# Kernel tuning notes

Hardware: AMD Instinct MI355X
Metric: run time of the kernel (lower is better)

## Reference

```python
import jax, jax.numpy as jnp
import numpy as np

N = 50000
E = 640000
IN_DIM = 128
HIDDEN = 128
OUT_DIM = 128


def setup_inputs() -> dict:
    key = jax.random.key(0)
    ks = jax.random.split(key, 8)
    x = jax.random.normal(ks[0], (N, IN_DIM), dtype=jnp.float32)
    edge_index = jax.random.randint(ks[1], (2, E), 0, N, dtype=jnp.int64)
    s = 1.0 / np.sqrt(IN_DIM)
    w1l = jax.random.uniform(ks[2], (HIDDEN, IN_DIM), minval=-s, maxval=s, dtype=jnp.float32)
    b1 = jax.random.uniform(ks[3], (HIDDEN,), minval=-s, maxval=s, dtype=jnp.float32)
    w1r = jax.random.uniform(ks[4], (HIDDEN, IN_DIM), minval=-s, maxval=s, dtype=jnp.float32)
    s2 = 1.0 / np.sqrt(HIDDEN)
    w2l = jax.random.uniform(ks[5], (OUT_DIM, HIDDEN), minval=-s2, maxval=s2, dtype=jnp.float32)
    b2 = jax.random.uniform(ks[6], (OUT_DIM,), minval=-s2, maxval=s2, dtype=jnp.float32)
    w2r = jax.random.uniform(ks[7], (OUT_DIM, HIDDEN), minval=-s2, maxval=s2, dtype=jnp.float32)
    return {"x": x, "edge_index": edge_index, "w1l": w1l, "b1": b1, "w1r": w1r,
            "w2l": w2l, "b2": b2, "w2r": w2r}


def sage_conv(x, src, dst, wl, bl, wr):
    # mean-aggregate source features at destination nodes
    msg = x[src]                                   # [E, d]
    agg = jax.ops.segment_sum(msg, dst, num_segments=N)   # [N, d]
    cnt = jax.ops.segment_sum(jnp.ones((src.shape[0],), x.dtype), dst, num_segments=N)
    agg = agg / jnp.maximum(cnt, 1.0)[:, None]
    # PyG SAGEConv: lin_l(agg) + lin_r(x); bias lives in lin_l
    return agg @ wl.T + bl + x @ wr.T


def reference(x, edge_index, w1l, b1, w1r, w2l, b2, w2r):
    src, dst = edge_index[0], edge_index[1]
    h = jax.nn.relu(sage_conv(x, src, dst, w1l, b1, w1r))
    out = sage_conv(h, src, dst, w2l, b2, w2r)
    return out
```

## Files before the change

### kernel.cpp

```cpp
#include <hip/hip_runtime.h>

#define DIM 128
#define CAP 64
#define FSTRIDE 16
#define PBLK 320

typedef _Float16 half8 __attribute__((ext_vector_type(8)));
typedef float floatx4 __attribute__((ext_vector_type(4)));
typedef unsigned short ushort8 __attribute__((ext_vector_type(8)));

__global__ void k_setup(const floatx4* __restrict__ in4, half8* __restrict__ out8,
                        const float* __restrict__ w1l, const float* __restrict__ w1r,
                        half8* __restrict__ Wf1,
                        const float* __restrict__ w2l, const float* __restrict__ w2r,
                        half8* __restrict__ Wf2,
                        const int* __restrict__ src, const int* __restrict__ dst,
                        int* __restrict__ fillS, unsigned short* __restrict__ pad,
                        int n8, int N, int E){
  int b = blockIdx.x;
  if (b < 8*PBLK){
    const int p = b & 7, c = b >> 3;
    const int PN = (N + 7) >> 3;
    const int n0 = p * PN;
    const int n1 = (n0 + PN < N) ? n0 + PN : N;
    const int CE = (E + PBLK - 1) / PBLK;
    const int e0 = c * CE;
    const int e1 = (e0 + CE < E) ? e0 + CE : E;
    for (int e = e0 + threadIdx.x; e < e1; e += 256){
      int d = dst[e];
      if (d >= n0 && d < n1){
        int s = src[e];
        int q = atomicAdd(&fillS[d*FSTRIDE], 1);
        if (q < CAP) pad[d*CAP + q] = (unsigned short)s;
      }
    }
  } else if (b < 8*PBLK + ((n8 + 255) >> 8)){
    int i = (b - 8*PBLK)*256 + threadIdx.x;
    if (i < n8){
      floatx4 a = in4[2*i], c = in4[2*i + 1];
      half8 h;
      h[0] = (_Float16)a[0]; h[1] = (_Float16)a[1];
      h[2] = (_Float16)a[2]; h[3] = (_Float16)a[3];
      h[4] = (_Float16)c[0]; h[5] = (_Float16)c[1];
      h[6] = (_Float16)c[2]; h[7] = (_Float16)c[3];
      out8[i] = h;
    }
  } else {
    int which = b - 8*PBLK - ((n8 + 255) >> 8);
    const float* wl = (which < 16) ? w1l : w2l;
    const float* wr = (which < 16) ? w1r : w2r;
    half8* Wf = (which < 16) ? Wf1 : Wf2;
    int t = (which & 15)*256 + threadIdx.x;
    int ks = t >> 9, jt = (t >> 6) & 7, lane = t & 63;
    int j = jt*16 + (lane & 15);
    int kb = ks*32 + (lane >> 4)*8;
    half8 h;
    #pragma unroll
    for (int i = 0; i < 8; ++i){
      int k = kb + i;
      float v = (k < 128) ? wl[j*128 + k] : wr[j*128 + (k - 128)];
      h[i] = (_Float16)v;
    }
    Wf[t] = h;
  }
}

__global__ __launch_bounds__(256) void k_agg(
    const half8* __restrict__ featH8, const unsigned short* __restrict__ pad,
    const int* __restrict__ fillS, half8* __restrict__ aggH8, int n)
{
  int node = blockIdx.x*16 + (threadIdx.x >> 4);
  int ch = threadIdx.x & 15;
  if (node >= n) return;
  int deg = fillS[node*FSTRIDE];
  int cnt = (deg < CAP) ? deg : CAP;
  const int base = node*CAP;
  float acc[8] = {0,0,0,0,0,0,0,0};
  for (int p = 0; p < cnt; p += 8){
    ushort8 si = *(const ushort8*)&pad[base + p];
    int   s[8];
    float w[8];
    #pragma unroll
    for (int u = 0; u < 8; ++u){
      bool valid = (p + u) < cnt;
      s[u] = valid ? (int)si[u] : 0;
      w[u] = valid ? 1.0f : 0.0f;
    }
    half8 v[8];
    #pragma unroll
    for (int u = 0; u < 8; ++u) v[u] = featH8[s[u]*16 + ch];
    #pragma unroll
    for (int u = 0; u < 8; ++u){
      #pragma unroll
      for (int i = 0; i < 8; ++i) acc[i] += w[u] * (float)v[u][i];
    }
  }
  float sc = 1.0f / fmaxf((float)deg, 1.0f);
  half8 o;
  #pragma unroll
  for (int i = 0; i < 8; ++i) o[i] = (_Float16)(acc[i]*sc);
  aggH8[node*16 + ch] = o;
}

template<bool RELU, bool OUT_HALF>
__global__ __launch_bounds__(256) void k_gemm(
    const half8* __restrict__ aggH8, const half8* __restrict__ selfH8,
    const half8* __restrict__ Wf, const float* __restrict__ bias,
    void* __restrict__ outp, int n)
{
  const int tid = threadIdx.x;
  const int lane = tid & 63, wv = tid >> 6;
  const int m = lane & 15, quad = lane >> 4;
  const int node0 = blockIdx.x * 64;
  const int arow = node0 + wv*16 + m;
  const int rowSafe = (arow < n) ? arow : 0;

  floatx4 acc[8] = {{0,0,0,0},{0,0,0,0},{0,0,0,0},{0,0,0,0},
                    {0,0,0,0},{0,0,0,0},{0,0,0,0},{0,0,0,0}};

  #pragma unroll
  for (int ks = 0; ks < 8; ++ks){
    half8 a = (ks < 4) ? aggH8 [rowSafe*16 + (ks    *4 + quad)]
                       : selfH8[rowSafe*16 + ((ks-4)*4 + quad)];
    if (arow >= n) a = half8{};
    #pragma unroll
    for (int jt = 0; jt < 8; ++jt){
      half8 b = Wf[(ks*8 + jt)*64 + lane];
      acc[jt] = __builtin_amdgcn_mfma_f32_16x16x32_f16(a, b, acc[jt], 0, 0, 0);
    }
  }

  #pragma unroll
  for (int jt = 0; jt < 8; ++jt){
    int j = jt*16 + m;
    float bj = bias[j];
    #pragma unroll
    for (int r = 0; r < 4; ++r){
      int node = node0 + wv*16 + quad*4 + r;
      if (node < n){
        float v = acc[jt][r] + bj;
        if (RELU) v = fmaxf(v, 0.f);
        if (OUT_HALF) ((_Float16*)outp)[node*DIM + j] = (_Float16)v;
        else          ((float*)outp)[node*DIM + j] = v;
      }
    }
  }
}

extern "C" void kernel_launch(void* const* d_in, const int* in_sizes, int n_in,
                              void* d_out, int out_size, void* d_ws, size_t ws_size,
                              hipStream_t stream)
{
  const float* x   = (const float*)d_in[0];
  const int*   ei  = (const int*)d_in[1];
  const float* w1l = (const float*)d_in[2];
  const float* b1  = (const float*)d_in[3];
  const float* w1r = (const float*)d_in[4];
  const float* w2l = (const float*)d_in[5];
  const float* b2  = (const float*)d_in[6];
  const float* w2r = (const float*)d_in[7];
  float* out = (float*)d_out;

  const int N = in_sizes[0] / DIM;
  const int E = in_sizes[1] / 2;

  char* p = (char*)d_ws;
  auto carve = [&](size_t bytes) -> char* {
    char* q = p;
    p += (bytes + 255) & ~(size_t)255;
    return q;
  };
  _Float16*       xh    = (_Float16*)carve((size_t)N * DIM * 2);
  _Float16*       hh    = (_Float16*)carve((size_t)N * DIM * 2);
  _Float16*       aggH  = (_Float16*)carve((size_t)N * DIM * 2);
  half8*          Wf1   = (half8*)carve(4096 * 16);
  half8*          Wf2   = (half8*)carve(4096 * 16);
  int*            fillS = (int*)carve((size_t)N * FSTRIDE * 4);
  unsigned short* pad   = (unsigned short*)carve((size_t)N * CAP * 2);

  const int* src = ei;
  const int* dst = ei + E;

  const int n8 = N * DIM / 8;
  const int bCast = (n8 + 255)/256;

  hipMemsetAsync(fillS, 0, (size_t)N * FSTRIDE * 4, stream);

  k_setup<<<8*PBLK + bCast + 32, 256, 0, stream>>>(
      (const floatx4*)x, (half8*)xh, w1l, w1r, Wf1, w2l, w2r, Wf2,
      src, dst, fillS, pad, n8, N, E);

  const int gAgg = (N + 15)/16;
  const int gGemm = (N + 63)/64;

  k_agg<<<gAgg, 256, 0, stream>>>((const half8*)xh, pad, fillS, (half8*)aggH, N);
  k_gemm<true, true><<<gGemm, 256, 0, stream>>>(
      (const half8*)aggH, (const half8*)xh, Wf1, b1, (void*)hh, N);
  k_agg<<<gAgg, 256, 0, stream>>>((const half8*)hh, pad, fillS, (half8*)aggH, N);
  k_gemm<false, false><<<gGemm, 256, 0, stream>>>(
      (const half8*)aggH, (const half8*)hh, Wf2, b2, (void*)out, N);
}
```

Before: 201.4 us.

## Fuse mean aggregation into MFMA GEMM via shared memory; vectorize edge bucketing

Merges the gather/mean aggregation kernel with the following MFMA GEMM. Each 128-thread block aggregates 32 nodes into an LDS tile, which then feeds the A operand for the first half of K. This removes the global round trip of the aggregate buffer and two kernel launches. Edge bucketing in setup now reads src/dst as int4 when the chunk is aligned. The smaller blocks and serial 4-group aggregation loop may reduce parallelism and latency hiding, and each block reloads the full weight matrix for only 32 rows.

New measurement: 214.2 us. 1.06x slower.

```diff
diff --git a/kernel.cpp b/kernel.cpp
--- a/kernel.cpp
+++ b/kernel.cpp
@@ -26,12 +26,36 @@
     const int CE = (E + PBLK - 1) / PBLK;
     const int e0 = c * CE;
     const int e1 = (e0 + CE < E) ? e0 + CE : E;
-    for (int e = e0 + threadIdx.x; e < e1; e += 256){
-      int d = dst[e];
-      if (d >= n0 && d < n1){
-        int s = src[e];
-        int q = atomicAdd(&fillS[d*FSTRIDE], 1);
-        if (q < CAP) pad[d*CAP + q] = (unsigned short)s;
+    if ((e0 & 3) == 0){
+      const int nvec = (e1 - e0) & ~3;
+      for (int eb = e0 + threadIdx.x*4; eb < e0 + nvec; eb += 1024){
+        int4 d4 = *(const int4*)(dst + eb);
+        int4 s4 = *(const int4*)(src + eb);
+        #pragma unroll
+        for (int u = 0; u < 4; ++u){
+          int d = (&d4.x)[u];
+          if (d >= n0 && d < n1){
+            int q = atomicAdd(&fillS[d*FSTRIDE], 1);
+            if (q < CAP) pad[d*CAP + q] = (unsigned short)((&s4.x)[u]);
+          }
+        }
+      }
+      for (int e = e0 + nvec + threadIdx.x; e < e1; e += 256){
+        int d = dst[e];
+        if (d >= n0 && d < n1){
+          int s = src[e];
+          int q = atomicAdd(&fillS[d*FSTRIDE], 1);
+          if (q < CAP) pad[d*CAP + q] = (unsigned short)s;
+        }
+      }
+    } else {
+      for (int e = e0 + threadIdx.x; e < e1; e += 256){
+        int d = dst[e];
+        if (d >= n0 && d < n1){
+          int s = src[e];
+          int q = atomicAdd(&fillS[d*FSTRIDE], 1);
+          if (q < CAP) pad[d*CAP + q] = (unsigned short)s;
+        }
       }
     }
   } else if (b < 8*PBLK + ((n8 + 255) >> 8)){
@@ -65,68 +89,76 @@
   }
 }
 
-__global__ __launch_bounds__(256) void k_agg(
+template<bool RELU, bool OUT_HALF>
+__global__ __launch_bounds__(128) void k_fused(
     const half8* __restrict__ featH8, const unsigned short* __restrict__ pad,
-    const int* __restrict__ fillS, half8* __restrict__ aggH8, int n)
+    const int* __restrict__ fillS, const half8* __restrict__ Wf,
+    const float* __restrict__ bias, void* __restrict__ outp, int n)
 {
-  int node = blockIdx.x*16 + (threadIdx.x >> 4);
-  int ch = threadIdx.x & 15;
-  if (node >= n) return;
-  int deg = fillS[node*FSTRIDE];
-  int cnt = (deg < CAP) ? deg : CAP;
-  const int base = node*CAP;
-  float acc[8] = {0,0,0,0,0,0,0,0};
-  for (int p = 0; p < cnt; p += 8){
-    ushort8 si = *(const ushort8*)&pad[base + p];
-    int   s[8];
-    float w[8];
-    #pragma unroll
-    for (int u = 0; u < 8; ++u){
-      bool valid = (p + u) < cnt;
-      s[u] = valid ? (int)si[u] : 0;
-      w[u] = valid ? 1.0f : 0.0f;
-    }
-    half8 v[8];
-    #pragma unroll
-    for (int u = 0; u < 8; ++u) v[u] = featH8[s[u]*16 + ch];
-    #pragma unroll
-    for (int u = 0; u < 8; ++u){
-      #pragma unroll
-      for (int i = 0; i < 8; ++i) acc[i] += w[u] * (float)v[u][i];
-    }
-  }
-  float sc = 1.0f / fmaxf((float)deg, 1.0f);
-  half8 o;
-  #pragma unroll
-  for (int i = 0; i < 8; ++i) o[i] = (_Float16)(acc[i]*sc);
-  aggH8[node*16 + ch] = o;
-}
-
-template<bool RELU, bool OUT_HALF>
-__global__ __launch_bounds__(256) void k_gemm(
-    const half8* __restrict__ aggH8, const half8* __restrict__ selfH8,
-    const half8* __restrict__ Wf, const float* __restrict__ bias,
-    void* __restrict__ outp, int n)
-{
+  __shared__ _Float16 aggL[32][136];
   const int tid = threadIdx.x;
+  const int node0 = blockIdx.x * 32;
+
+  const int ch = tid & 15;
+  const int mg = tid >> 4;
+  for (int g = 0; g < 4; ++g){
+    const int ml = g*8 + mg;
+    const int node = node0 + ml;
+    float acc[8] = {0,0,0,0,0,0,0,0};
+    float sc = 0.0f;
+    if (node < n){
+      int deg = fillS[node*FSTRIDE];
+      int cnt = (deg < CAP) ? deg : CAP;
+      const int base = node*CAP;
+      for (int p = 0; p < cnt; p += 8){
+        ushort8 si = *(const ushort8*)&pad[base + p];
+        int   s[8];
+        float w[8];
+        #pragma unroll
+        for (int u = 0; u < 8; ++u){
+          bool valid = (p + u) < cnt;
+          s[u] = valid ? (int)si[u] : 0;
+          w[u] = valid ? 1.0f : 0.0f;
+        }
+        half8 v[8];
+        #pragma unroll
+        for (int u = 0; u < 8; ++u) v[u] = featH8[s[u]*16 + ch];
+        #pragma unroll
+        for (int u = 0; u < 8; ++u){
+          #pragma unroll
+          for (int i = 0; i < 8; ++i) acc[i] += w[u] * (float)v[u][i];
+        }
+      }
+      sc = 1.0f / fmaxf((float)deg, 1.0f);
+    }
+    half8 o;
+    #pragma unroll
+    for (int i = 0; i < 8; ++i) o[i] = (_Float16)(acc[i]*sc);
+    *(half8*)&aggL[ml][ch*8] = o;
+  }
+  __syncthreads();
+
   const int lane = tid & 63, wv = tid >> 6;
   const int m = lane & 15, quad = lane >> 4;
-  const int node0 = blockIdx.x * 64;
   const int arow = node0 + wv*16 + m;
   const int rowSafe = (arow < n) ? arow : 0;
 
-  floatx4 acc[8] = {{0,0,0,0},{0,0,0,0},{0,0,0,0},{0,0,0,0},
-                    {0,0,0,0},{0,0,0,0},{0,0,0,0},{0,0,0,0}};
+  floatx4 acc2[8] = {{0,0,0,0},{0,0,0,0},{0,0,0,0},{0,0,0,0},
+                     {0,0,0,0},{0,0,0,0},{0,0,0,0},{0,0,0,0}};
 
   #pragma unroll
   for (int ks = 0; ks < 8; ++ks){
-    half8 a = (ks < 4) ? aggH8 [rowSafe*16 + (ks    *4 + quad)]
-                       : selfH8[rowSafe*16 + ((ks-4)*4 + quad)];
-    if (arow >= n) a = half8{};
+    half8 a;
+    if (ks < 4){
+      a = *(const half8*)&aggL[wv*16 + m][(ks*4 + quad)*8];
+    } else {
+      a = featH8[rowSafe*16 + (ks-4)*4 + quad];
+      if (arow >= n) a = half8{};
+    }
     #pragma unroll
     for (int jt = 0; jt < 8; ++jt){
-      half8 b = Wf[(ks*8 + jt)*64 + lane];
-      acc[jt] = __builtin_amdgcn_mfma_f32_16x16x32_f16(a, b, acc[jt], 0, 0, 0);
+      half8 bb = Wf[(ks*8 + jt)*64 + lane];
+      acc2[jt] = __builtin_amdgcn_mfma_f32_16x16x32_f16(a, bb, acc2[jt], 0, 0, 0);
     }
   }
 
@@ -138,7 +170,7 @@
     for (int r = 0; r < 4; ++r){
       int node = node0 + wv*16 + quad*4 + r;
       if (node < n){
-        float v = acc[jt][r] + bj;
+        float v = acc2[jt][r] + bj;
         if (RELU) v = fmaxf(v, 0.f);
         if (OUT_HALF) ((_Float16*)outp)[node*DIM + j] = (_Float16)v;
         else          ((float*)outp)[node*DIM + j] = v;
@@ -172,7 +204,6 @@
   };
   _Float16*       xh    = (_Float16*)carve((size_t)N * DIM * 2);
   _Float16*       hh    = (_Float16*)carve((size_t)N * DIM * 2);
-  _Float16*       aggH  = (_Float16*)carve((size_t)N * DIM * 2);
   half8*          Wf1   = (half8*)carve(4096 * 16);
   half8*          Wf2   = (half8*)carve(4096 * 16);
   int*            fillS = (int*)carve((size_t)N * FSTRIDE * 4);
@@ -190,13 +221,10 @@
       (const floatx4*)x, (half8*)xh, w1l, w1r, Wf1, w2l, w2r, Wf2,
       src, dst, fillS, pad, n8, N, E);
 
-  const int gAgg = (N + 15)/16;
-  const int gGemm = (N + 63)/64;
-
-  k_agg<<<gAgg, 256, 0, stream>>>((const half8*)xh, pad, fillS, (half8*)aggH, N);
-  k_gemm<true, true><<<gGemm, 256, 0, stream>>>(
-      (const half8*)aggH, (const half8*)xh, Wf1, b1, (void*)hh, N);
-  k_agg<<<gAgg, 256, 0, stream>>>((const half8*)hh, pad, fillS, (half8*)aggH, N);
-  k_gemm<false, false><<<gGemm, 256, 0, stream>>>(
-      (const half8*)aggH, (const half8*)hh, Wf2, b2, (void*)out, N);
+  const int gF = (N + 31)/32;
+
+  k_fused<true, true><<<gF, 128, 0, stream>>>(
+      (const half8*)xh, pad, fillS, Wf1, b1, (void*)hh, N);
+  k_fused<false, false><<<gF, 128, 0, stream>>>(
+      (const half8*)hh, pad, fillS, Wf2, b2, (void*)out, N);
 }
```
